# Kernel tuning notes

Measured on AMD Instinct MI355X. Metric: run time of the kernel, lower is better.

Reference implementation:

```python
import jax, jax.numpy as jnp
import numpy as np

D, H, E = 1024, 2048, 16  # input_dim, expert hidden (2*D), num_experts
B, S = 4, 2048
TEMP = 1.0
LN_EPS = 1e-5


def setup_inputs() -> dict:
    key = jax.random.key(0)
    ks = jax.random.split(key, 8)
    x = jax.random.normal(ks[0], (B, S, D), dtype=jnp.float32)
    router_w = 0.02 * jax.random.normal(ks[1], (E, D), dtype=jnp.float32)  # nn.Linear(D,E,bias=False)
    w1 = 0.02 * jax.random.normal(ks[2], (E, H, D), dtype=jnp.float32)     # torch Linear weight [out,in]
    b1 = jnp.zeros((E, H), dtype=jnp.float32)
    ln_g = jnp.ones((E, H), dtype=jnp.float32)
    ln_b = jnp.zeros((E, H), dtype=jnp.float32)
    w2 = 0.02 * jax.random.normal(ks[3], (E, D, H), dtype=jnp.float32)
    b2 = jnp.zeros((E, D), dtype=jnp.float32)
    return {"x": x, "router_w": router_w, "w1": w1, "b1": b1,
            "ln_g": ln_g, "ln_b": ln_b, "w2": w2, "b2": b2}


def reference(x, router_w, w1, b1, ln_g, ln_b, w2, b2):
    d = x.shape[-1]
    xf = x.reshape(-1, d)                       # [T, D]
    logits = (xf @ router_w.T) / TEMP           # [T, E]
    dispatch = jax.nn.softmax(logits, axis=0)   # softmax over tokens
    combine = jax.nn.softmax(logits, axis=-1)   # softmax over experts
    slots = dispatch.T @ xf                     # [E, D] one slot per expert
    # per-expert MLP, vectorized over E: Linear -> LayerNorm -> GELU -> Linear
    h = jnp.einsum('ed,ehd->eh', slots, w1) + b1          # [E, H]
    mu = h.mean(-1, keepdims=True)
    var = ((h - mu) ** 2).mean(-1, keepdims=True)         # biased var (torch LayerNorm)
    h = (h - mu) * jax.lax.rsqrt(var + LN_EPS) * ln_g + ln_b
    h = jax.nn.gelu(h, approximate=False)                 # nn.GELU exact erf
    slot_out = jnp.einsum('eh,edh->ed', h, w2) + b2       # [E, D]
    out = combine @ slot_out                              # [T, D]
    # router aux loss and entropy (eval-mode state subset)
    mean_usage = combine.mean(0)                          # [E]
    p = jax.nn.softmax(router_w.mean(-1), axis=0)         # [E]
    n_exp = router_w.shape[0]
    router_loss = n_exp * (mean_usage * p).sum()
    entropy = -(combine * jnp.log(combine + 1e-8)).sum(-1).mean()
    return out.reshape(x.shape), router_loss, entropy
```

## Files before the change

### kernel.cpp

```cpp
#include <hip/hip_runtime.h>
#include <hip/hip_bf16.h>
#include <math.h>

#define T_ 8192
#define D_ 1024
#define E_ 16
#define H_ 2048

typedef float f4 __attribute__((ext_vector_type(4)));

__device__ __forceinline__ float wave_sum(float v) {
    #pragma unroll
    for (int m = 32; m >= 1; m >>= 1) v += __shfl_xor(v, m, 64);
    return v;
}
__device__ __forceinline__ float wave_max(float v) {
    #pragma unroll
    for (int m = 32; m >= 1; m >>= 1) v = fmaxf(v, __shfl_xor(v, m, 64));
    return v;
}
__device__ __forceinline__ float grp16_sum(float v) {
    #pragma unroll
    for (int m = 8; m >= 1; m >>= 1) v += __shfl_xor(v, m, 16);
    return v;
}
__device__ __forceinline__ float grp16_max(float v) {
    #pragma unroll
    for (int m = 8; m >= 1; m >>= 1) v = fmaxf(v, __shfl_xor(v, m, 16));
    return v;
}

__global__ __launch_bounds__(256) void k1_logits_combine(const float* __restrict__ x,
                                                         const float* __restrict__ rw,
                                                         float* __restrict__ logits,
                                                         float* __restrict__ combine,
                                                         float* __restrict__ musum,
                                                         float* __restrict__ entacc) {
    __shared__ float rw_lds[E_ * D_];
    for (int i = threadIdx.x; i < E_ * D_; i += 256) rw_lds[i] = rw[i];
    __syncthreads();
    const int wave = threadIdx.x >> 6, lane = threadIdx.x & 63;
    const int t0 = blockIdx.x * 32 + wave * 8;
    const float4* rl = (const float4*)rw_lds;
    float mu_reg = 0.0f, ent_reg = 0.0f;
    for (int ti = 0; ti < 8; ++ti) {
        const int t = t0 + ti;
        const float4* xr = (const float4*)(x + (size_t)t * D_);
        float4 xv[4];
        #pragma unroll
        for (int k = 0; k < 4; ++k) xv[k] = xr[lane + 64 * k];
        float my = 0.0f;
        #pragma unroll
        for (int e = 0; e < E_; ++e) {
            float s = 0.0f;
            #pragma unroll
            for (int k = 0; k < 4; ++k) {
                float4 wv = rl[e * 256 + lane + 64 * k];
                s += xv[k].x * wv.x + xv[k].y * wv.y + xv[k].z * wv.z + xv[k].w * wv.w;
            }
            s = wave_sum(s);
            if (lane == e) my = s;
        }
        if (lane < E_) logits[(size_t)t * E_ + lane] = my;
        float m = grp16_max(my);
        float cexp = expf(my - m);
        float ssum = grp16_sum(cexp);
        float c = cexp / ssum;
        if (lane < E_) {
            combine[(size_t)t * E_ + lane] = c;
            mu_reg += c;
        }
        float entc = (lane < E_) ? (-c * logf(c + 1e-8f)) : 0.0f;
        entc = grp16_sum(entc);
        if (lane == 0) ent_reg += entc;
    }
    if (lane < E_) atomicAdd(&musum[lane], mu_reg);
    if (lane == 0) atomicAdd(entacc, ent_reg);
}

__global__ __launch_bounds__(256) void k2a_colstats(const float* __restrict__ logits,
                                                    float* __restrict__ colmax,
                                                    float* __restrict__ colsum) {
    const int e = blockIdx.x, tid = threadIdx.x;
    float m = -1e30f;
    for (int t = tid; t < T_; t += 256) m = fmaxf(m, logits[(size_t)t * E_ + e]);
    m = wave_max(m);
    __shared__ float red[4];
    if ((tid & 63) == 0) red[tid >> 6] = m;
    __syncthreads();
    m = fmaxf(fmaxf(red[0], red[1]), fmaxf(red[2], red[3]));
    __syncthreads();
    float s = 0.0f;
    for (int t = tid; t < T_; t += 256) s += expf(logits[(size_t)t * E_ + e] - m);
    s = wave_sum(s);
    if ((tid & 63) == 0) red[tid >> 6] = s;
    __syncthreads();
    if (tid == 0) {
        colmax[e] = m;
        colsum[e] = red[0] + red[1] + red[2] + red[3];
    }
}

__global__ __launch_bounds__(256) void k3_slots(const float* __restrict__ x,
                                                const float* __restrict__ logits,
                                                const float* __restrict__ colmax,
                                                const float* __restrict__ colsum,
                                                float* __restrict__ slots) {
    const int tid = threadIdx.x;
    __shared__ float disp[128 * E_];
    __shared__ float cm[E_], cs[E_];
    if (tid < E_) { cm[tid] = colmax[tid]; cs[tid] = 1.0f / colsum[tid]; }
    __syncthreads();
    const int t0 = blockIdx.y * 128;
    for (int idx = tid; idx < 128 * E_; idx += 256) {
        const int tt = idx >> 4, e = idx & 15;
        disp[idx] = expf(logits[(size_t)(t0 + tt) * E_ + e] - cm[e]) * cs[e];
    }
    __syncthreads();
    const int d = blockIdx.x * 256 + tid;
    float acc[E_];
    #pragma unroll
    for (int e = 0; e < E_; ++e) acc[e] = 0.0f;
    const float* xp = x + (size_t)t0 * D_ + d;
    for (int tt = 0; tt < 128; ++tt) {
        const float xv = xp[(size_t)tt * D_];
        const float4* dr = (const float4*)&disp[tt * E_];
        float4 d0 = dr[0], d1 = dr[1], d2 = dr[2], d3 = dr[3];
        acc[0]  += d0.x * xv; acc[1]  += d0.y * xv; acc[2]  += d0.z * xv; acc[3]  += d0.w * xv;
        acc[4]  += d1.x * xv; acc[5]  += d1.y * xv; acc[6]  += d1.z * xv; acc[7]  += d1.w * xv;
        acc[8]  += d2.x * xv; acc[9]  += d2.y * xv; acc[10] += d2.z * xv; acc[11] += d2.w * xv;
        acc[12] += d3.x * xv; acc[13] += d3.y * xv; acc[14] += d3.z * xv; acc[15] += d3.w * xv;
    }
    #pragma unroll
    for (int e = 0; e < E_; ++e) atomicAdd(&slots[e * D_ + d], acc[e]);
}

__global__ __launch_bounds__(256) void k4_h(const float* __restrict__ slots,
                                            const float* __restrict__ w1,
                                            const float* __restrict__ b1,
                                            float* __restrict__ h) {
    const int e = blockIdx.x >> 7;
    const int jgrp = (blockIdx.x & 127) * 16;
    const int wave = threadIdx.x >> 6, lane = threadIdx.x & 63;
    const float4* sr = (const float4*)(slots + e * D_);
    float4 sv[4];
    #pragma unroll
    for (int k = 0; k < 4; ++k) sv[k] = sr[lane + 64 * k];
    #pragma unroll
    for (int r = 0; r < 4; ++r) {
        const int j = jgrp + wave * 4 + r;
        const f4* wr = (const f4*)(w1 + ((size_t)e * H_ + j) * D_);
        float s = 0.0f;
        #pragma unroll
        for (int k = 0; k < 4; ++k) {
            f4 wv = __builtin_nontemporal_load(&wr[lane + 64 * k]);
            s += wv.x * sv[k].x + wv.y * sv[k].y + wv.z * sv[k].z + wv.w * sv[k].w;
        }
        s = wave_sum(s);
        if (lane == 0) h[e * H_ + j] = s + b1[e * H_ + j];
    }
}

__global__ __launch_bounds__(256) void k5_ln_gelu(const float* __restrict__ h,
                                                  const float* __restrict__ g,
                                                  const float* __restrict__ bb,
                                                  float* __restrict__ h2) {
    const int e = blockIdx.x, tid = threadIdx.x;
    float v[8];
    float s = 0.0f, ss = 0.0f;
    #pragma unroll
    for (int k = 0; k < 8; ++k) {
        v[k] = h[e * H_ + tid + 256 * k];
        s += v[k]; ss += v[k] * v[k];
    }
    s = wave_sum(s); ss = wave_sum(ss);
    __shared__ float rs[4], rss[4];
    if ((tid & 63) == 0) { rs[tid >> 6] = s; rss[tid >> 6] = ss; }
    __syncthreads();
    s = rs[0] + rs[1] + rs[2] + rs[3];
    ss = rss[0] + rss[1] + rss[2] + rss[3];
    const float mean = s * (1.0f / H_);
    const float var = ss * (1.0f / H_) - mean * mean;
    const float rstd = rsqrtf(var + 1e-5f);
    #pragma unroll
    for (int k = 0; k < 8; ++k) {
        const int i = tid + 256 * k;
        float y = (v[k] - mean) * rstd * g[e * H_ + i] + bb[e * H_ + i];
        h2[e * H_ + i] = 0.5f * y * (1.0f + erff(y * 0.70710678118654752f));
    }
}

__global__ __launch_bounds__(256) void k6_slotout(const float* __restrict__ h2,
                                                  const float* __restrict__ w2,
                                                  const float* __restrict__ b2,
                                                  float* __restrict__ slot_out) {
    const int e = blockIdx.x >> 6;
    const int dgrp = (blockIdx.x & 63) * 16;
    const int wave = threadIdx.x >> 6, lane = threadIdx.x & 63;
    const float4* hr = (const float4*)(h2 + e * H_);
    float4 hv[8];
    #pragma unroll
    for (int k = 0; k < 8; ++k) hv[k] = hr[lane + 64 * k];
    #pragma unroll
    for (int r = 0; r < 4; ++r) {
        const int d = dgrp + wave * 4 + r;
        const f4* wr = (const f4*)(w2 + ((size_t)e * D_ + d) * H_);
        float s = 0.0f;
        #pragma unroll
        for (int k = 0; k < 8; ++k) {
            f4 wv = __builtin_nontemporal_load(&wr[lane + 64 * k]);
            s += wv.x * hv[k].x + wv.y * hv[k].y + wv.z * hv[k].z + wv.w * hv[k].w;
        }
        s = wave_sum(s);
        if (lane == 0) slot_out[e * D_ + d] = s + b2[e * D_ + d];
    }
}

__global__ __launch_bounds__(256) void k7_out(const float* __restrict__ combine,
                                              const float* __restrict__ slot_out,
                                              float* __restrict__ out) {
    const int tbase = blockIdx.x * 16;
    __shared__ float cl[256];
    cl[threadIdx.x] = combine[(size_t)tbase * E_ + threadIdx.x];
    __syncthreads();
    float4 so[E_];
    const float4* sr = (const float4*)slot_out;
    #pragma unroll
    for (int e = 0; e < E_; ++e) so[e] = sr[e * 256 + threadIdx.x];
    for (int tt = 0; tt < 16; ++tt) {
        float4 acc = { 0.0f, 0.0f, 0.0f, 0.0f };
        #pragma unroll
        for (int e = 0; e < E_; ++e) {
            const float c = cl[tt * E_ + e];
            acc.x += c * so[e].x; acc.y += c * so[e].y;
            acc.z += c * so[e].z; acc.w += c * so[e].w;
        }
        ((float4*)out)[(size_t)(tbase + tt) * 256 + threadIdx.x] = acc;
    }
}

__global__ __launch_bounds__(256) void k8_scalars(const float* __restrict__ rw,
                                                  const float* __restrict__ musum,
                                                  const float* __restrict__ entacc,
                                                  float* __restrict__ out_scalars) {
    const int tid = threadIdx.x, lane = tid & 63, wave = tid >> 6;
    __shared__ float rm[E_];
    #pragma unroll
    for (int q = 0; q < 4; ++q) {
        const int e = wave * 4 + q;
        const float4* rr = (const float4*)(rw + e * D_);
        float s = 0.0f;
        #pragma unroll
        for (int k = 0; k < 4; ++k) {
            float4 v = rr[lane * 4 + k];
            s += v.x + v.y + v.z + v.w;
        }
        s = wave_sum(s);
        if (lane == 0) rm[e] = s * (1.0f / D_);
    }
    __syncthreads();
    if (tid == 0) {
        float m = rm[0];
        for (int e = 1; e < E_; ++e) m = fmaxf(m, rm[e]);
        float s = 0.0f, pe[E_];
        for (int e = 0; e < E_; ++e) { pe[e] = expf(rm[e] - m); s += pe[e]; }
        float loss = 0.0f;
        for (int e = 0; e < E_; ++e) loss += (musum[e] * (1.0f / T_)) * (pe[e] / s);
        loss *= (float)E_;
        out_scalars[0] = loss;
        out_scalars[1] = entacc[0] * (1.0f / T_);
    }
}

extern "C" void kernel_launch(void* const* d_in, const int* in_sizes, int n_in,
                              void* d_out, int out_size, void* d_ws, size_t ws_size,
                              hipStream_t stream) {
    const float* x    = (const float*)d_in[0];
    const float* rw   = (const float*)d_in[1];
    const float* w1   = (const float*)d_in[2];
    const float* b1   = (const float*)d_in[3];
    const float* ln_g = (const float*)d_in[4];
    const float* ln_b = (const float*)d_in[5];
    const float* w2   = (const float*)d_in[6];
    const float* b2   = (const float*)d_in[7];

    float* out = (float*)d_out;
    float* wsf = (float*)d_ws;

    float* logits   = wsf;
    float* combine  = wsf + 131072;
    float* colmax   = wsf + 262144;
    float* colsum   = wsf + 262160;
    float* h        = wsf + 262176;
    float* h2       = wsf + 294944;
    float* slot_out = wsf + 327712;
    float* slots    = wsf + 344096;
    float* musum    = wsf + 360480;
    float* entacc   = wsf + 360496;

    (void)hipMemsetAsync(slots, 0, (size_t)(16384 + 16 + 1) * sizeof(float), stream);

    k1_logits_combine<<<T_ / 32, 256, 0, stream>>>(x, rw, logits, combine, musum, entacc);
    k2a_colstats<<<E_, 256, 0, stream>>>(logits, colmax, colsum);
    k3_slots<<<dim3(4, 64), 256, 0, stream>>>(x, logits, colmax, colsum, slots);
    k4_h<<<E_ * 128, 256, 0, stream>>>(slots, w1, b1, h);
    k5_ln_gelu<<<E_, 256, 0, stream>>>(h, ln_g, ln_b, h2);
    k6_slotout<<<E_ * 64, 256, 0, stream>>>(h2, w2, b2, slot_out);
    k7_out<<<T_ / 16, 256, 0, stream>>>(combine, slot_out, out);
    k8_scalars<<<1, 256, 0, stream>>>(rw, musum, entacc, out + (size_t)T_ * D_);
}
```

Before: 388.7 us.

## Fuse column stats, LayerNorm/GELU and scalars into neighbouring kernels

```diff
diff --git a/kernel.cpp b/kernel.cpp
--- a/kernel.cpp
+++ b/kernel.cpp
@@ -14,11 +14,6 @@
     for (int m = 32; m >= 1; m >>= 1) v += __shfl_xor(v, m, 64);
     return v;
 }
-__device__ __forceinline__ float wave_max(float v) {
-    #pragma unroll
-    for (int m = 32; m >= 1; m >>= 1) v = fmaxf(v, __shfl_xor(v, m, 64));
-    return v;
-}
 __device__ __forceinline__ float grp16_sum(float v) {
     #pragma unroll
     for (int m = 8; m >= 1; m >>= 1) v += __shfl_xor(v, m, 16);
@@ -34,87 +29,63 @@
                                                          const float* __restrict__ rw,
                                                          float* __restrict__ logits,
                                                          float* __restrict__ combine,
+                                                         float* __restrict__ colsum,
                                                          float* __restrict__ musum,
                                                          float* __restrict__ entacc) {
     __shared__ float rw_lds[E_ * D_];
     for (int i = threadIdx.x; i < E_ * D_; i += 256) rw_lds[i] = rw[i];
     __syncthreads();
-    const int wave = threadIdx.x >> 6, lane = threadIdx.x & 63;
-    const int t0 = blockIdx.x * 32 + wave * 8;
-    const float4* rl = (const float4*)rw_lds;
-    float mu_reg = 0.0f, ent_reg = 0.0f;
-    for (int ti = 0; ti < 8; ++ti) {
-        const int t = t0 + ti;
-        const float4* xr = (const float4*)(x + (size_t)t * D_);
-        float4 xv[4];
-        #pragma unroll
-        for (int k = 0; k < 4; ++k) xv[k] = xr[lane + 64 * k];
-        float my = 0.0f;
-        #pragma unroll
-        for (int e = 0; e < E_; ++e) {
-            float s = 0.0f;
-            #pragma unroll
-            for (int k = 0; k < 4; ++k) {
-                float4 wv = rl[e * 256 + lane + 64 * k];
-                s += xv[k].x * wv.x + xv[k].y * wv.y + xv[k].z * wv.z + xv[k].w * wv.w;
-            }
-            s = wave_sum(s);
-            if (lane == e) my = s;
-        }
-        if (lane < E_) logits[(size_t)t * E_ + lane] = my;
-        float m = grp16_max(my);
-        float cexp = expf(my - m);
-        float ssum = grp16_sum(cexp);
-        float c = cexp / ssum;
-        if (lane < E_) {
-            combine[(size_t)t * E_ + lane] = c;
-            mu_reg += c;
-        }
-        float entc = (lane < E_) ? (-c * logf(c + 1e-8f)) : 0.0f;
-        entc = grp16_sum(entc);
-        if (lane == 0) ent_reg += entc;
-    }
-    if (lane < E_) atomicAdd(&musum[lane], mu_reg);
-    if (lane == 0) atomicAdd(entacc, ent_reg);
-}
-
-__global__ __launch_bounds__(256) void k2a_colstats(const float* __restrict__ logits,
-                                                    float* __restrict__ colmax,
-                                                    float* __restrict__ colsum) {
-    const int e = blockIdx.x, tid = threadIdx.x;
-    float m = -1e30f;
-    for (int t = tid; t < T_; t += 256) m = fmaxf(m, logits[(size_t)t * E_ + e]);
-    m = wave_max(m);
-    __shared__ float red[4];
-    if ((tid & 63) == 0) red[tid >> 6] = m;
-    __syncthreads();
-    m = fmaxf(fmaxf(red[0], red[1]), fmaxf(red[2], red[3]));
-    __syncthreads();
-    float s = 0.0f;
-    for (int t = tid; t < T_; t += 256) s += expf(logits[(size_t)t * E_ + e] - m);
-    s = wave_sum(s);
-    if ((tid & 63) == 0) red[tid >> 6] = s;
-    __syncthreads();
-    if (tid == 0) {
-        colmax[e] = m;
-        colsum[e] = red[0] + red[1] + red[2] + red[3];
-    }
+    const int lane = threadIdx.x & 63, wave = threadIdx.x >> 6;
+    const int grp = lane >> 4, l16 = lane & 15;
+    const int t = blockIdx.x * 16 + wave * 4 + grp;
+    const f4* xr = (const f4*)(x + (size_t)t * D_);
+    f4 xv[16];
+    #pragma unroll
+    for (int k = 0; k < 16; ++k) xv[k] = xr[l16 + 16 * k];
+    const f4* rl = (const f4*)rw_lds;
+    float my = 0.0f;
+    #pragma unroll
+    for (int e = 0; e < E_; ++e) {
+        float s = 0.0f;
+        #pragma unroll
+        for (int k = 0; k < 16; ++k) {
+            f4 wv = rl[e * 256 + l16 + 16 * k];
+            s += wv.x * xv[k].x + wv.y * xv[k].y + wv.z * xv[k].z + wv.w * xv[k].w;
+        }
+        s = grp16_sum(s);
+        if (l16 == e) my = s;
+    }
+    logits[(size_t)t * E_ + l16] = my;
+    float m = grp16_max(my);
+    float cexp = expf(my - m);
+    float ssum = grp16_sum(cexp);
+    float c = cexp / ssum;
+    combine[(size_t)t * E_ + l16] = c;
+    float ce = expf(my);
+    float ent = -c * logf(c + 1e-8f);
+    float entt = grp16_sum(ent);
+    float mu = c;  mu += __shfl_xor(mu, 16, 64);  mu += __shfl_xor(mu, 32, 64);
+    float cs = ce; cs += __shfl_xor(cs, 16, 64);  cs += __shfl_xor(cs, 32, 64);
+    float et = entt; et += __shfl_xor(et, 16, 64); et += __shfl_xor(et, 32, 64);
+    if (lane < E_) {
+        atomicAdd(&musum[l16], mu);
+        atomicAdd(&colsum[l16], cs);
+    }
+    if (lane == 0) atomicAdd(entacc, et);
 }
 
 __global__ __launch_bounds__(256) void k3_slots(const float* __restrict__ x,
                                                 const float* __restrict__ logits,
-                                                const float* __restrict__ colmax,
                                                 const float* __restrict__ colsum,
                                                 float* __restrict__ slots) {
     const int tid = threadIdx.x;
-    __shared__ float disp[128 * E_];
-    __shared__ float cm[E_], cs[E_];
-    if (tid < E_) { cm[tid] = colmax[tid]; cs[tid] = 1.0f / colsum[tid]; }
-    __syncthreads();
-    const int t0 = blockIdx.y * 128;
-    for (int idx = tid; idx < 128 * E_; idx += 256) {
-        const int tt = idx >> 4, e = idx & 15;
-        disp[idx] = expf(logits[(size_t)(t0 + tt) * E_ + e] - cm[e]) * cs[e];
+    __shared__ float disp[64 * E_];
+    __shared__ float cs[E_];
+    if (tid < E_) cs[tid] = 1.0f / colsum[tid];
+    __syncthreads();
+    const int t0 = blockIdx.y * 64;
+    for (int idx = tid; idx < 64 * E_; idx += 256) {
+        disp[idx] = expf(logits[(size_t)t0 * E_ + idx]) * cs[idx & 15];
     }
     __syncthreads();
     const int d = blockIdx.x * 256 + tid;
@@ -122,7 +93,7 @@
     #pragma unroll
     for (int e = 0; e < E_; ++e) acc[e] = 0.0f;
     const float* xp = x + (size_t)t0 * D_ + d;
-    for (int tt = 0; tt < 128; ++tt) {
+    for (int tt = 0; tt < 64; ++tt) {
         const float xv = xp[(size_t)tt * D_];
         const float4* dr = (const float4*)&disp[tt * E_];
         float4 d0 = dr[0], d1 = dr[1], d2 = dr[2], d3 = dr[3];
@@ -138,12 +109,45 @@
 __global__ __launch_bounds__(256) void k4_h(const float* __restrict__ slots,
                                             const float* __restrict__ w1,
                                             const float* __restrict__ b1,
-                                            float* __restrict__ h) {
+                                            float* __restrict__ h,
+                                            const float* __restrict__ rw,
+                                            const float* __restrict__ musum,
+                                            const float* __restrict__ entacc,
+                                            float* __restrict__ out_scalars) {
+    const int wave = threadIdx.x >> 6, lane = threadIdx.x & 63;
+    if (blockIdx.x == E_ * 128) {
+        const int tid = threadIdx.x;
+        __shared__ float rm[E_];
+        #pragma unroll
+        for (int q = 0; q < 4; ++q) {
+            const int e = wave * 4 + q;
+            const f4* rr = (const f4*)(rw + e * D_);
+            float s = 0.0f;
+            #pragma unroll
+            for (int k = 0; k < 4; ++k) {
+                f4 v = rr[lane * 4 + k];
+                s += v.x + v.y + v.z + v.w;
+            }
+            s = wave_sum(s);
+            if (lane == 0) rm[e] = s * (1.0f / D_);
+        }
+        __syncthreads();
+        if (tid == 0) {
+            float m = rm[0];
+            for (int e = 1; e < E_; ++e) m = fmaxf(m, rm[e]);
+            float s = 0.0f, pe[E_];
+            for (int e = 0; e < E_; ++e) { pe[e] = expf(rm[e] - m); s += pe[e]; }
+            float loss = 0.0f;
+            for (int e = 0; e < E_; ++e) loss += (musum[e] * (1.0f / T_)) * (pe[e] / s);
+            out_scalars[0] = loss * (float)E_;
+            out_scalars[1] = entacc[0] * (1.0f / T_);
+        }
+        return;
+    }
     const int e = blockIdx.x >> 7;
     const int jgrp = (blockIdx.x & 127) * 16;
-    const int wave = threadIdx.x >> 6, lane = threadIdx.x & 63;
-    const float4* sr = (const float4*)(slots + e * D_);
-    float4 sv[4];
+    const f4* sr = (const f4*)(slots + e * D_);
+    f4 sv[4];
     #pragma unroll
     for (int k = 0; k < 4; ++k) sv[k] = sr[lane + 64 * k];
     #pragma unroll
@@ -161,58 +165,52 @@
     }
 }
 
-__global__ __launch_bounds__(256) void k5_ln_gelu(const float* __restrict__ h,
+__global__ __launch_bounds__(256) void k6_slotout(const float* __restrict__ h,
                                                   const float* __restrict__ g,
                                                   const float* __restrict__ bb,
-                                                  float* __restrict__ h2) {
-    const int e = blockIdx.x, tid = threadIdx.x;
-    float v[8];
-    float s = 0.0f, ss = 0.0f;
-    #pragma unroll
-    for (int k = 0; k < 8; ++k) {
-        v[k] = h[e * H_ + tid + 256 * k];
-        s += v[k]; ss += v[k] * v[k];
-    }
-    s = wave_sum(s); ss = wave_sum(ss);
-    __shared__ float rs[4], rss[4];
-    if ((tid & 63) == 0) { rs[tid >> 6] = s; rss[tid >> 6] = ss; }
-    __syncthreads();
-    s = rs[0] + rs[1] + rs[2] + rs[3];
-    ss = rss[0] + rss[1] + rss[2] + rss[3];
-    const float mean = s * (1.0f / H_);
-    const float var = ss * (1.0f / H_) - mean * mean;
-    const float rstd = rsqrtf(var + 1e-5f);
-    #pragma unroll
-    for (int k = 0; k < 8; ++k) {
-        const int i = tid + 256 * k;
-        float y = (v[k] - mean) * rstd * g[e * H_ + i] + bb[e * H_ + i];
-        h2[e * H_ + i] = 0.5f * y * (1.0f + erff(y * 0.70710678118654752f));
-    }
-}
-
-__global__ __launch_bounds__(256) void k6_slotout(const float* __restrict__ h2,
                                                   const float* __restrict__ w2,
                                                   const float* __restrict__ b2,
                                                   float* __restrict__ slot_out) {
     const int e = blockIdx.x >> 6;
     const int dgrp = (blockIdx.x & 63) * 16;
     const int wave = threadIdx.x >> 6, lane = threadIdx.x & 63;
-    const float4* hr = (const float4*)(h2 + e * H_);
-    float4 hv[8];
-    #pragma unroll
-    for (int k = 0; k < 8; ++k) hv[k] = hr[lane + 64 * k];
+    const f4* hr = (const f4*)(h + e * H_);
+    f4 hv[8];
+    float s = 0.0f, ss = 0.0f;
+    #pragma unroll
+    for (int k = 0; k < 8; ++k) {
+        hv[k] = hr[lane + 64 * k];
+        s  += hv[k].x + hv[k].y + hv[k].z + hv[k].w;
+        ss += hv[k].x * hv[k].x + hv[k].y * hv[k].y + hv[k].z * hv[k].z + hv[k].w * hv[k].w;
+    }
+    s = wave_sum(s); ss = wave_sum(ss);
+    const float mean = s * (1.0f / H_);
+    const float var = ss * (1.0f / H_) - mean * mean;
+    const float rstd = rsqrtf(var + 1e-5f);
+    const f4* gr = (const f4*)(g + e * H_);
+    const f4* br = (const f4*)(bb + e * H_);
+    #pragma unroll
+    for (int k = 0; k < 8; ++k) {
+        f4 g4 = gr[lane + 64 * k];
+        f4 b4 = br[lane + 64 * k];
+        float y;
+        y = (hv[k].x - mean) * rstd * g4.x + b4.x; hv[k].x = 0.5f * y * (1.0f + erff(y * 0.70710678118654752f));
+        y = (hv[k].y - mean) * rstd * g4.y + b4.y; hv[k].y = 0.5f * y * (1.0f + erff(y * 0.70710678118654752f));
+        y = (hv[k].z - mean) * rstd * g4.z + b4.z; hv[k].z = 0.5f * y * (1.0f + erff(y * 0.70710678118654752f));
+        y = (hv[k].w - mean) * rstd * g4.w + b4.w; hv[k].w = 0.5f * y * (1.0f + erff(y * 0.70710678118654752f));
+    }
     #pragma unroll
     for (int r = 0; r < 4; ++r) {
         const int d = dgrp + wave * 4 + r;
         const f4* wr = (const f4*)(w2 + ((size_t)e * D_ + d) * H_);
-        float s = 0.0f;
+        float acc = 0.0f;
         #pragma unroll
         for (int k = 0; k < 8; ++k) {
             f4 wv = __builtin_nontemporal_load(&wr[lane + 64 * k]);
-            s += wv.x * hv[k].x + wv.y * hv[k].y + wv.z * hv[k].z + wv.w * hv[k].w;
-        }
-        s = wave_sum(s);
-        if (lane == 0) slot_out[e * D_ + d] = s + b2[e * D_ + d];
+            acc += wv.x * hv[k].x + wv.y * hv[k].y + wv.z * hv[k].z + wv.w * hv[k].w;
+        }
+        acc = wave_sum(acc);
+        if (lane == 0) slot_out[e * D_ + d] = acc + b2[e * D_ + d];
     }
 }
 
@@ -236,39 +234,6 @@
             acc.z += c * so[e].z; acc.w += c * so[e].w;
         }
         ((float4*)out)[(size_t)(tbase + tt) * 256 + threadIdx.x] = acc;
-    }
-}
-
-__global__ __launch_bounds__(256) void k8_scalars(const float* __restrict__ rw,
-                                                  const float* __restrict__ musum,
-                                                  const float* __restrict__ entacc,
-                                                  float* __restrict__ out_scalars) {
-    const int tid = threadIdx.x, lane = tid & 63, wave = tid >> 6;
-    __shared__ float rm[E_];
-    #pragma unroll
-    for (int q = 0; q < 4; ++q) {
-        const int e = wave * 4 + q;
-        const float4* rr = (const float4*)(rw + e * D_);
-        float s = 0.0f;
-        #pragma unroll
-        for (int k = 0; k < 4; ++k) {
-            float4 v = rr[lane * 4 + k];
-            s += v.x + v.y + v.z + v.w;
-        }
-        s = wave_sum(s);
-        if (lane == 0) rm[e] = s * (1.0f / D_);
-    }
-    __syncthreads();
-    if (tid == 0) {
-        float m = rm[0];
-        for (int e = 1; e < E_; ++e) m = fmaxf(m, rm[e]);
-        float s = 0.0f, pe[E_];
-        for (int e = 0; e < E_; ++e) { pe[e] = expf(rm[e] - m); s += pe[e]; }
-        float loss = 0.0f;
-        for (int e = 0; e < E_; ++e) loss += (musum[e] * (1.0f / T_)) * (pe[e] / s);
-        loss *= (float)E_;
-        out_scalars[0] = loss;
-        out_scalars[1] = entacc[0] * (1.0f / T_);
     }
 }
 
@@ -289,23 +254,18 @@
 
     float* logits   = wsf;
     float* combine  = wsf + 131072;
-    float* colmax   = wsf + 262144;
-    float* colsum   = wsf + 262160;
-    float* h        = wsf + 262176;
-    float* h2       = wsf + 294944;
-    float* slot_out = wsf + 327712;
-    float* slots    = wsf + 344096;
-    float* musum    = wsf + 360480;
-    float* entacc   = wsf + 360496;
-
-    (void)hipMemsetAsync(slots, 0, (size_t)(16384 + 16 + 1) * sizeof(float), stream);
-
-    k1_logits_combine<<<T_ / 32, 256, 0, stream>>>(x, rw, logits, combine, musum, entacc);
-    k2a_colstats<<<E_, 256, 0, stream>>>(logits, colmax, colsum);
-    k3_slots<<<dim3(4, 64), 256, 0, stream>>>(x, logits, colmax, colsum, slots);
-    k4_h<<<E_ * 128, 256, 0, stream>>>(slots, w1, b1, h);
-    k5_ln_gelu<<<E_, 256, 0, stream>>>(h, ln_g, ln_b, h2);
-    k6_slotout<<<E_ * 64, 256, 0, stream>>>(h2, w2, b2, slot_out);
+    float* h        = wsf + 262144;
+    float* slot_out = wsf + 294912;
+    float* slots    = wsf + 311296;
+    float* colsum   = wsf + 327680;
+    float* musum    = wsf + 327696;
+    float* entacc   = wsf + 327712;
+
+    (void)hipMemsetAsync(slots, 0, (size_t)(16384 + 16 + 16 + 1) * sizeof(float), stream);
+
+    k1_logits_combine<<<T_ / 16, 256, 0, stream>>>(x, rw, logits, combine, colsum, musum, entacc);
+    k3_slots<<<dim3(4, 128), 256, 0, stream>>>(x, logits, colsum, slots);
+    k4_h<<<E_ * 128 + 1, 256, 0, stream>>>(slots, w1, b1, h, rw, musum, entacc, out + (size_t)T_ * D_);
+    k6_slotout<<<E_ * 64, 256, 0, stream>>>(h, ln_g, ln_b, w2, b2, slot_out);
     k7_out<<<T_ / 16, 256, 0, stream>>>(combine, slot_out, out);
-    k8_scalars<<<1, 256, 0, stream>>>(rw, musum, entacc, out + (size_t)T_ * D_);
-}
+}
```

After: 368.2 us. -5.3%, faster.
